# Optimization experiments

Measured on AMD Instinct MI355X. Metric: run time of the kernel, lower is better.

## Reference

```python
import jax, jax.numpy as jnp
import numpy as np

N, D, B = 8192, 16, 4
F_EMB, F_FEAT, F_ENC, H, HID = 32, 4, 128, 4, 64
GRAPH_LAYERS, FLOW_ITERS, DUAL_ITERS = 2, 20, 20
DUAL_STEP, DUAL_MOM = 0.01, 0.9


def _graph():
    # symmetric circulant graph: offsets {1,N-1,2,N-2,...}; reverse of slot 2i is 2i+1
    offs = np.array([o for k in range(1, D // 2 + 1) for o in (k, N - k)], dtype=np.int32)
    rev = np.arange(D, dtype=np.int32).reshape(-1, 2)[:, ::-1].reshape(-1)
    v = np.arange(N, dtype=np.int32)[:, None]
    adj = (v + offs[None, :]) % N          # out-neighbor of node v at slot d
    in_nbr = (v - offs[None, :]) % N       # source node of in-edge to v stored at slot d
    out_flat = adj * D + rev[None, :]      # flat index of reverse edge in [N*D]
    bcast = lambda a: np.broadcast_to(a[None], (B, N, D)).copy()
    return bcast(adj), bcast(in_nbr), bcast(out_flat)


def setup_inputs() -> dict:
    key = jax.random.key(0)
    ks = iter(jax.random.split(key, 32))
    dense = lambda k, fi, fo: jax.random.normal(k, (fi, fo), jnp.float32) / np.sqrt(fi)
    adj, in_nbr, out_flat = _graph()
    demands = jax.random.normal(next(ks), (B, N, 1), jnp.float32)
    demands = demands - jnp.mean(demands, axis=1, keepdims=True)  # net-zero supply/demand
    return dict(
        node_embeddings=jax.random.normal(next(ks), (B, N, F_EMB), jnp.float32),
        node_features=jax.random.uniform(next(ks), (B, N, F_FEAT), jnp.float32),
        demands=demands,
        adj_lst=jnp.asarray(adj), flow_indices=jnp.asarray(in_nbr),
        out_indices=jnp.asarray(out_flat), num_nodes=N,
        enc_W1=dense(next(ks), F_EMB + F_FEAT, HID), enc_b1=jnp.zeros((HID,), jnp.float32),
        enc_W2=dense(next(ks), HID, F_ENC), enc_b2=jnp.zeros((F_ENC,), jnp.float32),
        attn_W=jax.random.normal(next(ks), (H, F_ENC, F_ENC), jnp.float32) / np.sqrt(F_ENC),
        attn_aq=jax.random.normal(next(ks), (H, F_ENC), jnp.float32) / np.sqrt(F_ENC),
        attn_ak=jax.random.normal(next(ks), (H, F_ENC), jnp.float32) / np.sqrt(F_ENC),
        gru_W=dense(next(ks), F_ENC, 3 * F_ENC), gru_U=dense(next(ks), F_ENC, 3 * F_ENC),
        gru_b=jnp.zeros((3 * F_ENC,), jnp.float32),
        dec_W1=dense(next(ks), F_ENC, HID), dec_b1=jnp.zeros((HID,), jnp.float32),
        dec_W2=dense(next(ks), HID, 1), dec_b2=jnp.zeros((1,), jnp.float32),
        dual_W1=dense(next(ks), F_ENC, HID), dual_b1=jnp.zeros((HID,), jnp.float32),
        dual_W2=dense(next(ks), HID, 1), dual_b2=jnp.zeros((1,), jnp.float32),
    )


def _mlp2(x, W1, b1, W2, b2, activate_final):
    h = jnp.tanh(x @ W1 + b1)
    o = h @ W2 + b2
    return jnp.tanh(o) if activate_final else o


def _attention_neighborhood(x, adj, W, aq, ak):
    # x:[B,N,F], adj:[B,N,D]; multi-head attention over adjacency-list neighbors
    cq = jnp.einsum('bnf,hf->bhn', x, jnp.einsum('hfg,hg->hf', W, aq))
    ck = jnp.einsum('bnf,hf->bhn', x, jnp.einsum('hfg,hg->hf', W, ak))
    ck_nb = jax.vmap(lambda c, a: c[:, a])(ck, adj)           # [B,H,N,D]
    attn = jax.nn.softmax(jnp.tanh(cq[..., None] + ck_nb), axis=-1)
    x_nb = jax.vmap(lambda xb, a: xb[a])(x, adj)              # [B,N,D,F]
    weighted = jnp.einsum('bhnd,bndf->bhnf', attn, x_nb)
    out = jnp.tanh(jnp.mean(jnp.einsum('bhnf,hfg->bhng', weighted, W), axis=1))
    return out, attn


def _gru(x, h, W, U, b):
    gz, gr, gc = jnp.split(x @ W + b, 3, axis=-1)
    Uz, Ur, Uc = jnp.split(U, 3, axis=1)
    z = jax.nn.sigmoid(gz + h @ Uz)
    r = jax.nn.sigmoid(gr + h @ Ur)
    c = jnp.tanh(gc + (r * h) @ Uc)
    return z * h + (1.0 - z) * c


def _cost(x):
    return x * x


def _cost_deriv(x):
    return 2.0 * x


def _mcf(w, demand, in_idx):
    # proportional min-cost-flow iteration; in_idx[b,v,d] = source of in-edge at slot d
    flow0 = w * jax.nn.relu(-demand)
    def step(carry, _):
        flow, _ = carry
        inflow = jnp.sum(jnp.take_along_axis(flow, in_idx, axis=1), axis=-1, keepdims=True)
        new = w * jax.nn.relu(inflow - demand)
        return (new, flow), None
    (flow, pflow), _ = jax.lax.scan(step, (flow0, flow0), None, length=FLOW_ITERS)
    return flow, pflow


def _dual_flow(dual_diff, mask):
    # projected momentum descent on cost(f) - dual_diff*f, f >= 0
    z = jnp.zeros_like(dual_diff)
    def step(carry, _):
        flow, acc = carry
        deriv = _cost_deriv(flow - DUAL_MOM * acc) - dual_diff
        acc2 = DUAL_MOM * acc + DUAL_STEP * deriv
        flow2 = jax.nn.relu(mask * (flow - acc2))
        return (flow2, acc2), None
    (flow, _), _ = jax.lax.scan(step, (z, z), None, length=DUAL_ITERS)
    return flow


def reference(node_embeddings, node_features, demands, adj_lst, flow_indices, out_indices,
              num_nodes, enc_W1, enc_b1, enc_W2, enc_b2, attn_W, attn_aq, attn_ak,
              gru_W, gru_U, gru_b, dec_W1, dec_b1, dec_W2, dec_b2,
              dual_W1, dual_b1, dual_W2, dual_b2):
    h = _mlp2(jnp.concatenate([node_embeddings, node_features], axis=-1),
              enc_W1, enc_b1, enc_W2, enc_b2, True)
    for _ in range(GRAPH_LAYERS):  # layers share weights (tf AUTO_REUSE)
        nxt, _ = _attention_neighborhood(h, adj_lst, attn_W, attn_aq, attn_ak)
        h = _gru(nxt, h, gru_W, gru_U, gru_b)
    node_w = _mlp2(h, dec_W1, dec_b1, dec_W2, dec_b2, False)       # [B,N,1]
    pred = jax.vmap(lambda w, a: w[a, 0])(node_w, adj_lst)         # [B,N,D]
    mask = (adj_lst != num_nodes).astype(pred.dtype)
    norm_w = jax.nn.softmax(pred, axis=-1)
    flow, _ = _mcf(norm_w, demands, flow_indices)
    # flow correction: cancel opposing flow on reverse edges
    bf = flow.reshape(B, N * D)
    rev = jnp.take_along_axis(bf, out_indices.reshape(B, N * D), axis=1).reshape(flow.shape)
    flow = jax.nn.relu(flow - jnp.minimum(flow, rev))
    flow_cost = jnp.sum(_cost(flow), axis=(1, 2))
    dual_vars = _mlp2(h, dual_W1, dual_b1, dual_W2, dual_b2, False)  # [B,N,1]
    dual = mask * dual_vars
    dual_tr = mask * jax.vmap(lambda w, a: w[a, 0])(dual_vars, adj_lst)
    dual_diff = dual - dual_tr
    dual_flows = _dual_flow(dual_diff, mask)
    dual_demand = jnp.sum(dual_vars * demands, axis=(1, 2))
    dual_cost = jnp.sum(_cost(dual_flows) - dual_diff * dual_flows, axis=(1, 2)) - dual_demand
    return flow_cost - dual_cost  # loss, [B]
```

## Files before the change

### kernel.cpp

```cpp
#include <hip/hip_runtime.h>

#define NN 8192
#define BB 4
#define DD 16

typedef unsigned short ushort_t;
typedef short bf16x8 __attribute__((ext_vector_type(8)));
typedef float f32x4 __attribute__((ext_vector_type(4)));
typedef unsigned short u16x4 __attribute__((ext_vector_type(4)));
typedef unsigned short u16x8 __attribute__((ext_vector_type(8)));

__host__ __device__ constexpr int soff(int d) { return (d & 1) ? -((d >> 1) + 1) : ((d >> 1) + 1); }

__device__ __forceinline__ float sigmoidf(float x) { return 1.f / (1.f + expf(-x)); }

__device__ __forceinline__ unsigned short f2b(float f) {
  union { float f; unsigned int u; } x;
  x.f = f;
  unsigned int r = (x.u + 0x7FFFu + ((x.u >> 16) & 1u)) >> 16;
  return (unsigned short)r;
}
__device__ __forceinline__ float b2f(ushort_t v) {
  union { unsigned int u; float f; } x;
  x.u = ((unsigned int)v) << 16;
  return x.f;
}

__device__ __forceinline__ float wave_sum(float v) {
#pragma unroll
  for (int o = 32; o; o >>= 1) v += __shfl_down(v, o, 64);
  return v;
}

__global__ __launch_bounds__(256) void prep_kernel(
    const float* __restrict__ gW, const float* __restrict__ gU, const float* __restrict__ aW,
    const float* __restrict__ eW1, const float* __restrict__ eW2,
    const float* __restrict__ dW1, const float* __restrict__ uW1,
    ushort_t* __restrict__ Wt, ushort_t* __restrict__ Wt3, ushort_t* __restrict__ Wt2,
    ushort_t* __restrict__ W1f, ushort_t* __restrict__ W2f,
    ushort_t* __restrict__ dW1f, ushort_t* __restrict__ uW1f) {
  int i = blockIdx.x * 256 + threadIdx.x;
  if (i < 98304) {
    int e = i & 7, lane = (i >> 3) & 63, ks = (i >> 9) & 7, nt = i >> 12;
    int m = lane & 15, g = lane >> 4;
    int n = nt * 16 + m, k = ks * 32 + g * 8 + e;
    float v;
    if (k < 128) v = gW[k * 384 + n];
    else v = (n < 256) ? gU[(k - 128) * 384 + n] : 0.f;
    Wt[i] = f2b(v);
  } else if (i < 114688) {
    int j = i - 98304;
    int e = j & 7, lane = (j >> 3) & 63, ks = (j >> 9) & 3, nt = j >> 11;
    int m = lane & 15, g = lane >> 4;
    int n = nt * 16 + m, k = ks * 32 + g * 8 + e;
    Wt3[j] = f2b(gU[k * 384 + 256 + n]);
  } else if (i < 180224) {
    int j = i - 114688;
    int e = j & 7, lane = (j >> 3) & 63, ks = (j >> 9) & 15, nt = j >> 13;
    int m = lane & 15, g = lane >> 4;
    int gc = nt * 16 + m, k = ks * 32 + g * 8 + e;
    int hh = k >> 7, f = k & 127;
    Wt2[j] = f2b(aW[hh * 16384 + f * 128 + gc]);
  } else if (i < 184320) {
    int j = i - 180224;
    int e = j & 7, lane = (j >> 3) & 63, ks = (j >> 9) & 1, nt = j >> 10;
    int m = lane & 15, g = lane >> 4;
    int n = nt * 16 + m, k = ks * 32 + g * 8 + e;
    W1f[j] = f2b(k < 36 ? eW1[k * 64 + n] : 0.f);
  } else if (i < 192512) {
    int j = i - 184320;
    int e = j & 7, lane = (j >> 3) & 63, ks = (j >> 9) & 1, nt = j >> 10;
    int m = lane & 15, g = lane >> 4;
    int n = nt * 16 + m, k = ks * 32 + g * 8 + e;
    W2f[j] = f2b(eW2[k * 128 + n]);
  } else if (i < 200704) {
    int j = i - 192512;
    int e = j & 7, lane = (j >> 3) & 63, ks = (j >> 9) & 3, nt = j >> 11;
    int m = lane & 15, g = lane >> 4;
    int n = nt * 16 + m, k = ks * 32 + g * 8 + e;
    dW1f[j] = f2b(dW1[k * 64 + n]);
  } else if (i < 208896) {
    int j = i - 200704;
    int e = j & 7, lane = (j >> 3) & 63, ks = (j >> 9) & 3, nt = j >> 11;
    int m = lane & 15, g = lane >> 4;
    int n = nt * 16 + m, k = ks * 32 + g * 8 + e;
    uW1f[j] = f2b(uW1[k * 64 + n]);
  }
}

#define EBS 72
__global__ __launch_bounds__(256) void enc_kernel(
    const float* __restrict__ emb, const float* __restrict__ feat,
    const ushort_t* __restrict__ W1f, const float* __restrict__ b1,
    const ushort_t* __restrict__ W2f, const float* __restrict__ b2,
    ushort_t* __restrict__ hout) {
  __shared__ alignas(16) ushort_t embB[64 * EBS];
  __shared__ alignas(16) ushort_t hidB[64 * EBS];
  int tid = threadIdx.x;
  int w = tid >> 6, lane = tid & 63, m = lane & 15, g = lane >> 4;
  size_t n0 = (size_t)blockIdx.x * 64;
  f32x4 z4 = {0.f, 0.f, 0.f, 0.f};
#pragma unroll
  for (int i = 0; i < 9; i++) ((unsigned int*)embB)[tid + i * 256] = 0u;
  __syncthreads();
#pragma unroll
  for (int i = 0; i < 2; i++) {
    int idx = tid + i * 256;
    int r = idx >> 3, c4 = (idx & 7) * 4;
    float4 v = *(const float4*)&emb[(n0 + r) * 32 + c4];
    u16x4 q = {f2b(v.x), f2b(v.y), f2b(v.z), f2b(v.w)};
    *(u16x4*)&embB[r * EBS + c4] = q;
  }
  if (tid < 64) {
    float4 v = *(const float4*)&feat[(n0 + tid) * 4];
    u16x4 q = {f2b(v.x), f2b(v.y), f2b(v.z), f2b(v.w)};
    *(u16x4*)&embB[tid * EBS + 32] = q;
  }
  __syncthreads();
  {
    f32x4 acc[4];
#pragma unroll
    for (int nt = 0; nt < 4; nt++) acc[nt] = z4;
#pragma unroll
    for (int ks = 0; ks < 2; ks++) {
      bf16x8 a = *(const bf16x8*)&embB[(w * 16 + m) * EBS + ks * 32 + g * 8];
#pragma unroll
      for (int nt = 0; nt < 4; nt++) {
        bf16x8 bb = *(const bf16x8*)&W1f[((nt * 2 + ks) * 64 + lane) * 8];
        acc[nt] = __builtin_amdgcn_mfma_f32_16x16x32_bf16(a, bb, acc[nt], 0, 0, 0);
      }
    }
#pragma unroll
    for (int nt = 0; nt < 4; nt++) {
      int col = nt * 16 + m;
      float bv = b1[col];
#pragma unroll
      for (int r = 0; r < 4; r++)
        hidB[(w * 16 + g * 4 + r) * EBS + col] = f2b(tanhf(acc[nt][r] + bv));
    }
  }
  __syncthreads();
  {
    f32x4 acc[8];
#pragma unroll
    for (int nt = 0; nt < 8; nt++) acc[nt] = z4;
#pragma unroll
    for (int ks = 0; ks < 2; ks++) {
      bf16x8 a = *(const bf16x8*)&hidB[(w * 16 + m) * EBS + ks * 32 + g * 8];
#pragma unroll
      for (int nt = 0; nt < 8; nt++) {
        bf16x8 bb = *(const bf16x8*)&W2f[((nt * 2 + ks) * 64 + lane) * 8];
        acc[nt] = __builtin_amdgcn_mfma_f32_16x16x32_bf16(a, bb, acc[nt], 0, 0, 0);
      }
    }
#pragma unroll
    for (int nt = 0; nt < 8; nt++) {
      int col = nt * 16 + m;
      float bv = b2[col];
#pragma unroll
      for (int r = 0; r < 4; r++)
        hout[(n0 + w * 16 + g * 4 + r) * 128 + col] = f2b(tanhf(acc[nt][r] + bv));
    }
  }
}

__global__ __launch_bounds__(256) void aqw_kernel(
    const float* __restrict__ W, const float* __restrict__ aq, const float* __restrict__ ak,
    ushort_t* __restrict__ aqkB, float* __restrict__ acc) {
  int i = blockIdx.x * 256 + threadIdx.x;
  if (blockIdx.x == 9 && threadIdx.x < BB) acc[threadIdx.x] = 0.f;
  if (i < 512) {
    int hh = i >> 7, f = i & 127;
    const float* w = W + ((size_t)hh * 128 + f) * 128;
    float s = 0.f, s2 = 0.f;
    for (int g = 0; g < 128; g++) {
      s += w[g] * aq[hh * 128 + g];
      s2 += w[g] * ak[hh * 128 + g];
    }
    int ks = f >> 5, g = (f >> 3) & 3, e = f & 7;
    aqkB[(ks * 64 + g * 16 + hh) * 8 + e] = f2b(s2);
    aqkB[(ks * 64 + g * 16 + 4 + hh) * 8 + e] = f2b(s);
  } else if (i < 2560) {
    int j = i - 512;
    int lane = (j >> 3) & 63;
    if ((lane & 15) >= 8) aqkB[j] = 0;
  }
}

#define HBS 136
#define FRB 528
#define FRW 264
__global__ __launch_bounds__(256, 4) void layer_kernel(
    const ushort_t* __restrict__ hin, const ushort_t* __restrict__ Wt2,
    const ushort_t* __restrict__ Wt, const ushort_t* __restrict__ Wt3,
    const ushort_t* __restrict__ aqkB,
    const float* __restrict__ bg, ushort_t* __restrict__ hout) {
  __shared__ alignas(16) ushort_t hl_bf[32 * HBS];
  __shared__ alignas(16) ushort_t hlT_u[4352];
  __shared__ float ckl[32 * 5];
  __shared__ float cql[16 * 5];
  __shared__ alignas(16) ushort_t aexp[4 * FRB];
  __shared__ alignas(16) ushort_t wgB[16 * FRB];
  ushort_t* hlT = hlT_u;
  ushort_t* xB = hlT_u;
  ushort_t* rhB = hlT_u + 16 * HBS;
  int b = blockIdx.y, v0 = blockIdx.x * 16, tid = threadIdx.x;
  int w = tid >> 6, lane = tid & 63, m = lane & 15, g = lane >> 4;
  const ushort_t* hb = hin + (size_t)b * NN * 128;
  size_t base = ((size_t)b * NN + v0) * 128;
  f32x4 z4 = {0.f, 0.f, 0.f, 0.f};
#pragma unroll
  for (int i = 0; i < 2; i++) {
    int idx = tid + i * 256;
    int r = idx >> 4, c8 = (idx & 15) * 8;
    int row = (v0 - 8 + r) & (NN - 1);
    *(u16x8*)&hl_bf[r * HBS + c8] = *(const u16x8*)&hb[(size_t)row * 128 + c8];
  }
#pragma unroll
  for (int i = 0; i < 4; i++) {
    int word = tid + i * 256;
    ((unsigned int*)aexp)[(word >> 8) * FRW + (word & 255)] = 0u;
  }
  __syncthreads();
#pragma unroll
  for (int i = 0; i < 4; i++) {
    int idx = tid + i * 256;
    int c = idx & 127, r4 = (idx >> 7) * 4;
    u16x4 q = {hl_bf[r4 * HBS + c], hl_bf[(r4 + 1) * HBS + c],
               hl_bf[(r4 + 2) * HBS + c], hl_bf[(r4 + 3) * HBS + c]};
    *(u16x4*)&hlT[(c >> 4) * FRB + (((r4 >> 3)) * 16 + (c & 15)) * 8 + (r4 & 7)] = q;
  }
  if (w < 2) {
    f32x4 accB = z4;
    for (int ks = 0; ks < 4; ks++) {
      bf16x8 a = *(const bf16x8*)&hl_bf[(w * 16 + m) * HBS + ks * 32 + g * 8];
      bf16x8 bb = *(const bf16x8*)&aqkB[(ks * 64 + lane) * 8];
      accB = __builtin_amdgcn_mfma_f32_16x16x32_bf16(a, bb, accB, 0, 0, 0);
    }
    int arow = w * 16 + g * 4;
    if (m < 4) {
#pragma unroll
      for (int r = 0; r < 4; r++) ckl[(arow + r) * 5 + m] = accB[r];
    } else if (m < 8) {
#pragma unroll
      for (int r = 0; r < 4; r++) {
        int row = arow + r;
        if (row >= 8 && row < 24) cql[(row - 8) * 5 + (m - 4)] = accB[r];
      }
    }
  }
  __syncthreads();
  {
    int grp = tid >> 2, q = tid & 3;
    int t = grp >> 2, hh = grp & 3;
    float cq = cql[t * 5 + hh];
    float ex[4];
    float mx = -3.0e38f;
#pragma unroll
    for (int dq = 0; dq < 4; dq++) {
      int d = q * 4 + dq;
      float s = tanhf(cq + ckl[(t + 8 + soff(d)) * 5 + hh]);
      ex[dq] = s;
      mx = fmaxf(mx, s);
    }
    mx = fmaxf(mx, __shfl_xor(mx, 1, 64));
    mx = fmaxf(mx, __shfl_xor(mx, 2, 64));
    float sum = 0.f;
#pragma unroll
    for (int dq = 0; dq < 4; dq++) {
      ex[dq] = expf(ex[dq] - mx);
      sum += ex[dq];
    }
    sum += __shfl_xor(sum, 1, 64);
    sum += __shfl_xor(sum, 2, 64);
    float inv = 1.f / sum;
#pragma unroll
    for (int dq = 0; dq < 4; dq++) {
      int d = q * 4 + dq;
      int col = t + 8 + soff(d);
      aexp[hh * FRB + ((col >> 3) * 16 + t) * 8 + (col & 7)] = f2b(ex[dq] * inv);
    }
  }
  __syncthreads();
  {
    bf16x8 bwin[2];
#pragma unroll
    for (int t2 = 0; t2 < 2; t2++)
      bwin[t2] = *(const bf16x8*)&hlT[(w * 2 + t2) * FRB + lane * 8];
#pragma unroll
    for (int hh = 0; hh < 4; hh++) {
      bf16x8 a = *(const bf16x8*)&aexp[hh * FRB + lane * 8];
#pragma unroll
      for (int t2 = 0; t2 < 2; t2++) {
        int nt = w * 2 + t2;
        f32x4 c = __builtin_amdgcn_mfma_f32_16x16x32_bf16(a, bwin[t2], z4, 0, 0, 0);
        int ksb = hh * 4 + (nt >> 1);
        int gq = (nt & 1) * 2 + (m >> 3);
        int e = m & 7;
#pragma unroll
        for (int r = 0; r < 4; r++)
          wgB[ksb * FRB + (gq * 16 + g * 4 + r) * 8 + e] = f2b(c[r]);
      }
    }
  }
  __syncthreads();
  {
    f32x4 acc[2];
    acc[0] = z4; acc[1] = z4;
    for (int ks = 0; ks < 16; ks++) {
      bf16x8 a = *(const bf16x8*)&wgB[ks * FRB + lane * 8];
#pragma unroll
      for (int t2 = 0; t2 < 2; t2++) {
        int nt = w * 2 + t2;
        bf16x8 bb = *(const bf16x8*)&Wt2[((nt * 16 + ks) * 64 + lane) * 8];
        acc[t2] = __builtin_amdgcn_mfma_f32_16x16x32_bf16(a, bb, acc[t2], 0, 0, 0);
      }
    }
    __syncthreads();
#pragma unroll
    for (int t2 = 0; t2 < 2; t2++) {
      int gc = (w * 2 + t2) * 16 + m;
#pragma unroll
      for (int r = 0; r < 4; r++)
        xB[(g * 4 + r) * HBS + gc] = f2b(tanhf(0.25f * acc[t2][r]));
    }
  }
  __syncthreads();
  f32x4 accZ[2], accR[2], accG[2];
#pragma unroll
  for (int t2 = 0; t2 < 2; t2++) { accZ[t2] = z4; accR[t2] = z4; accG[t2] = z4; }
  for (int ks = 0; ks < 8; ks++) {
    bf16x8 a = (ks < 4) ? *(const bf16x8*)&xB[m * HBS + ks * 32 + g * 8]
                        : *(const bf16x8*)&hl_bf[(m + 8) * HBS + (ks - 4) * 32 + g * 8];
#pragma unroll
    for (int t2 = 0; t2 < 2; t2++) {
      int ntz = w * 2 + t2;
      bf16x8 bz = *(const bf16x8*)&Wt[((ntz * 8 + ks) * 64 + lane) * 8];
      accZ[t2] = __builtin_amdgcn_mfma_f32_16x16x32_bf16(a, bz, accZ[t2], 0, 0, 0);
      bf16x8 br = *(const bf16x8*)&Wt[(((8 + ntz) * 8 + ks) * 64 + lane) * 8];
      accR[t2] = __builtin_amdgcn_mfma_f32_16x16x32_bf16(a, br, accR[t2], 0, 0, 0);
      if (ks < 4) {
        bf16x8 bc = *(const bf16x8*)&Wt[(((16 + ntz) * 8 + ks) * 64 + lane) * 8];
        accG[t2] = __builtin_amdgcn_mfma_f32_16x16x32_bf16(a, bc, accG[t2], 0, 0, 0);
      }
    }
  }
  float zf[2][4], gcf[2][4];
#pragma unroll
  for (int t2 = 0; t2 < 2; t2++) {
    int j = (w * 2 + t2) * 16 + m;
    float bz = bg[j], br = bg[128 + j], bc = bg[256 + j];
#pragma unroll
    for (int r = 0; r < 4; r++) {
      int row = g * 4 + r;
      float hv = b2f(hl_bf[(row + 8) * HBS + j]);
      zf[t2][r] = sigmoidf(accZ[t2][r] + bz);
      float rr = sigmoidf(accR[t2][r] + br);
      rhB[row * HBS + j] = f2b(rr * hv);
      gcf[t2][r] = accG[t2][r] + bc;
    }
  }
  __syncthreads();
  ushort_t* hstage = wgB;
  {
    f32x4 acc2[2];
    acc2[0] = z4; acc2[1] = z4;
    for (int ks = 0; ks < 4; ks++) {
      bf16x8 a = *(const bf16x8*)&rhB[m * HBS + ks * 32 + g * 8];
#pragma unroll
      for (int t2 = 0; t2 < 2; t2++) {
        int nt = w * 2 + t2;
        bf16x8 bb = *(const bf16x8*)&Wt3[((nt * 4 + ks) * 64 + lane) * 8];
        acc2[t2] = __builtin_amdgcn_mfma_f32_16x16x32_bf16(a, bb, acc2[t2], 0, 0, 0);
      }
    }
#pragma unroll
    for (int t2 = 0; t2 < 2; t2++) {
      int j = (w * 2 + t2) * 16 + m;
#pragma unroll
      for (int r = 0; r < 4; r++) {
        int row = g * 4 + r;
        float hv = b2f(hl_bf[(row + 8) * HBS + j]);
        float c = tanhf(gcf[t2][r] + acc2[t2][r]);
        hstage[row * HBS + j] = f2b(zf[t2][r] * hv + (1.f - zf[t2][r]) * c);
      }
    }
  }
  __syncthreads();
  {
    int row = tid >> 4, c8 = (tid & 15) * 8;
    *(u16x8*)&hout[base + (size_t)row * 128 + c8] = *(const u16x8*)&hstage[row * HBS + c8];
  }
}

__global__ __launch_bounds__(256) void dec_kernel(
    const ushort_t* __restrict__ h, const float* __restrict__ dem,
    const ushort_t* __restrict__ dW1f, const float* __restrict__ db1,
    const float* __restrict__ dW2, const float* __restrict__ db2,
    const ushort_t* __restrict__ uW1f, const float* __restrict__ ub1,
    const float* __restrict__ uW2, const float* __restrict__ ub2,
    float* __restrict__ node_w, float* __restrict__ dual_v, float* __restrict__ acc) {
  __shared__ alignas(16) ushort_t hB[64 * HBS];
  __shared__ float red[4];
  int b = blockIdx.y, n0 = blockIdx.x * 64, tid = threadIdx.x;
  int w = tid >> 6, lane = tid & 63, m = lane & 15, g = lane >> 4;
  f32x4 z4 = {0.f, 0.f, 0.f, 0.f};
  size_t base = ((size_t)b * NN + n0) * 128;
#pragma unroll
  for (int i = 0; i < 4; i++) {
    int idx = tid + i * 256;
    int r = idx >> 4, c8 = (idx & 15) * 8;
    *(u16x8*)&hB[r * HBS + c8] = *(const u16x8*)&h[base + (size_t)r * 128 + c8];
  }
  __syncthreads();
  f32x4 accD[4], accU[4];
#pragma unroll
  for (int nt = 0; nt < 4; nt++) { accD[nt] = z4; accU[nt] = z4; }
  for (int ks = 0; ks < 4; ks++) {
    bf16x8 a = *(const bf16x8*)&hB[(w * 16 + m) * HBS + ks * 32 + g * 8];
#pragma unroll
    for (int nt = 0; nt < 4; nt++) {
      bf16x8 bd = *(const bf16x8*)&dW1f[((nt * 4 + ks) * 64 + lane) * 8];
      accD[nt] = __builtin_amdgcn_mfma_f32_16x16x32_bf16(a, bd, accD[nt], 0, 0, 0);
      bf16x8 bu = *(const bf16x8*)&uW1f[((nt * 4 + ks) * 64 + lane) * 8];
      accU[nt] = __builtin_amdgcn_mfma_f32_16x16x32_bf16(a, bu, accU[nt], 0, 0, 0);
    }
  }
  float accd = 0.f;
#pragma unroll
  for (int r = 0; r < 4; r++) {
    float sD = 0.f, sU = 0.f;
#pragma unroll
    for (int nt = 0; nt < 4; nt++) {
      int col = nt * 16 + m;
      sD += tanhf(accD[nt][r] + db1[col]) * dW2[col];
      sU += tanhf(accU[nt][r] + ub1[col]) * uW2[col];
    }
#pragma unroll
    for (int o = 1; o < 16; o <<= 1) {
      sD += __shfl_xor(sD, o, 64);
      sU += __shfl_xor(sU, o, 64);
    }
    if (m == 0) {
      int n = n0 + w * 16 + g * 4 + r;
      node_w[(size_t)b * NN + n] = sD + db2[0];
      float dv = sU + ub2[0];
      dual_v[(size_t)b * NN + n] = dv;
      accd += dv * dem[(size_t)b * NN + n];
    }
  }
  float s = wave_sum(accd);
  if (lane == 0) red[w] = s;
  __syncthreads();
  if (tid == 0) atomicAdd(&acc[b], red[0] + red[1] + red[2] + red[3]);
}

__global__ __launch_bounds__(64) void sm_kernel(
    const float* __restrict__ node_w, const float* __restrict__ dem,
    float* __restrict__ nwT, float* __restrict__ fl0) {
  int b = blockIdx.y;
  int v = blockIdx.x * 64 + threadIdx.x;
  const float* nw = node_w + (size_t)b * NN;
  float p[16];
  float mx = -3.0e38f;
#pragma unroll
  for (int d = 0; d < 16; d++) {
    p[d] = nw[(v + soff(d)) & (NN - 1)];
    mx = fmaxf(mx, p[d]);
  }
  float s = 0.f;
#pragma unroll
  for (int d = 0; d < 16; d++) {
    p[d] = expf(p[d] - mx);
    s += p[d];
  }
  float inv = 1.f / s;
  float fd = fmaxf(-dem[(size_t)b * NN + v], 0.f);
#pragma unroll
  for (int d = 0; d < 16; d++) {
    size_t idx = ((size_t)b * 16 + d) * NN + v;
    float w = p[d] * inv;
    nwT[idx] = w;
    fl0[idx] = w * fd;
  }
}

#define MCI 10
#define MHALO 80
#define MCW 128
#define MCOLS (MCW + 2 * MHALO)
__global__ __launch_bounds__(256) void mcf_fused_kernel(
    const float* __restrict__ src, float* __restrict__ dstg,
    const float* __restrict__ nwT, const float* __restrict__ dem) {
  __shared__ float fl[2][16][MCOLS];
  __shared__ float dm[MCOLS];
  int b = blockIdx.y, v0 = blockIdx.x * MCW, tid = threadIdx.x;
  for (int e = tid; e < 16 * MCOLS; e += 256) {
    int d = e / MCOLS, c = e - d * MCOLS;
    int g = (v0 - MHALO + c) & (NN - 1);
    fl[0][d][c] = src[((size_t)b * 16 + d) * NN + g];
  }
  for (int c = tid; c < MCOLS; c += 256)
    dm[c] = dem[(size_t)b * NN + ((v0 - MHALO + c) & (NN - 1))];
  __syncthreads();
  int cur = 0;
  for (int it = 0; it < MCI; it++) {
    int lo = 8 * (it + 1), hi = MCOLS - 8 * (it + 1);
    for (int c = lo + tid; c < hi; c += 256) {
      float s = 0.f;
#pragma unroll
      for (int d = 0; d < 16; d++) s += fl[cur][d][c - soff(d)];
      float val = fmaxf(s - dm[c], 0.f);
      int g = (v0 - MHALO + c) & (NN - 1);
#pragma unroll
      for (int d = 0; d < 16; d++)
        fl[1 - cur][d][c] = nwT[((size_t)b * 16 + d) * NN + g] * val;
    }
    cur ^= 1;
    __syncthreads();
  }
  if (tid < MCW) {
    int c = MHALO + tid;
    int g = v0 + tid;
#pragma unroll
    for (int d = 0; d < 16; d++)
      dstg[((size_t)b * 16 + d) * NN + g] = fl[cur][d][c];
  }
}

__global__ __launch_bounds__(64) void tail_kernel(
    const float* __restrict__ fl, const float* __restrict__ dv, float* __restrict__ acc) {
  int b = blockIdx.y;
  int v = blockIdx.x * 64 + threadIdx.x;
  float s = 0.f;
#pragma unroll
  for (int d = 0; d < 16; d++) {
    float f = fl[((size_t)b * 16 + d) * NN + v];
    int a = (v + soff(d)) & (NN - 1);
    float r = fl[((size_t)b * 16 + (d ^ 1)) * NN + a];
    float c = f - fminf(f, r);
    c = fmaxf(c, 0.f);
    s += c * c;
  }
  float me = dv[(size_t)b * NN + v];
#pragma unroll
  for (int d = 0; d < 16; d++) {
    float dd = me - dv[(size_t)b * NN + ((v + soff(d)) & (NN - 1))];
    float f = 0.f, ac = 0.f;
#pragma unroll
    for (int it = 0; it < 20; it++) {
      float deriv = 2.f * (f - 0.9f * ac) - dd;
      ac = 0.9f * ac + 0.01f * deriv;
      f = fmaxf(f - ac, 0.f);
    }
    s -= f * f - dd * f;
  }
  s = wave_sum(s);
  if (threadIdx.x == 0) atomicAdd(&acc[b], s);
}

__global__ __launch_bounds__(64) void fin_kernel(const float* __restrict__ acc, float* __restrict__ out) {
  int i = threadIdx.x;
  if (i < BB) out[i] = acc[i];
}
__global__ __launch_bounds__(64) void sentinel_kernel(float* __restrict__ out) {
  int i = threadIdx.x;
  if (i < BB) out[i] = 99999.0f;
}

extern "C" void kernel_launch(void* const* d_in, const int* in_sizes, int n_in,
                              void* d_out, int out_size, void* d_ws, size_t ws_size,
                              hipStream_t stream) {
  (void)out_size; (void)ws_size;
  float* out = (float*)d_out;
  if (n_in < 25 || in_sizes[0] != 1048576 || in_sizes[3] != 524288 ||
      in_sizes[11] != 65536 || in_sizes[14] != 49152 || in_sizes[24] != 1) {
    sentinel_kernel<<<dim3(1), 64, 0, stream>>>(out);
    return;
  }
  const float* emb = (const float*)d_in[0];
  const float* feat = (const float*)d_in[1];
  const float* dem = (const float*)d_in[2];
  const float* eW1 = (const float*)d_in[7];
  const float* eb1 = (const float*)d_in[8];
  const float* eW2 = (const float*)d_in[9];
  const float* eb2 = (const float*)d_in[10];
  const float* aW = (const float*)d_in[11];
  const float* aq = (const float*)d_in[12];
  const float* ak = (const float*)d_in[13];
  const float* gW = (const float*)d_in[14];
  const float* gU = (const float*)d_in[15];
  const float* gb = (const float*)d_in[16];
  const float* dW1 = (const float*)d_in[17];
  const float* db1 = (const float*)d_in[18];
  const float* dW2 = (const float*)d_in[19];
  const float* db2 = (const float*)d_in[20];
  const float* uW1 = (const float*)d_in[21];
  const float* ub1 = (const float*)d_in[22];
  const float* uW2 = (const float*)d_in[23];
  const float* ub2 = (const float*)d_in[24];

  float* ws = (float*)d_ws;
  ushort_t* h = (ushort_t*)ws;
  ushort_t* h2 = h + 4194304;
  float* aqkBf = ws + 4194304;
  float* node_w = aqkBf + 1024;
  float* dualv = node_w + 32768;
  float* nwT = dualv + 32768;
  float* flA = nwT + 524288;
  float* flB = flA + 524288;
  float* accv = flB + 524288;
  ushort_t* aqkB = (ushort_t*)aqkBf;
  ushort_t* Wt = (ushort_t*)nwT;
  ushort_t* Wt3 = Wt + 98304;
  ushort_t* Wt2 = Wt3 + 16384;
  ushort_t* W1f = Wt2 + 65536;
  ushort_t* W2f = W1f + 4096;
  ushort_t* dW1f = W2f + 8192;
  ushort_t* uW1f = dW1f + 8192;

  aqw_kernel<<<dim3(10), 256, 0, stream>>>(aW, aq, ak, aqkB, accv);
  prep_kernel<<<dim3(816), 256, 0, stream>>>(gW, gU, aW, eW1, eW2, dW1, uW1,
                                             Wt, Wt3, Wt2, W1f, W2f, dW1f, uW1f);
  enc_kernel<<<dim3(512), 256, 0, stream>>>(emb, feat, W1f, eb1, W2f, eb2, h);
  layer_kernel<<<dim3(512, 4), 256, 0, stream>>>(h, Wt2, Wt, Wt3, aqkB, gb, h2);
  layer_kernel<<<dim3(512, 4), 256, 0, stream>>>(h2, Wt2, Wt, Wt3, aqkB, gb, h);
  dec_kernel<<<dim3(128, 4), 256, 0, stream>>>(h, dem, dW1f, db1, dW2, db2,
                                               uW1f, ub1, uW2, ub2, node_w, dualv, accv);
  sm_kernel<<<dim3(128, 4), 64, 0, stream>>>(node_w, dem, nwT, flA);
  mcf_fused_kernel<<<dim3(64, 4), 256, 0, stream>>>(flA, flB, nwT, dem);
  mcf_fused_kernel<<<dim3(64, 4), 256, 0, stream>>>(flB, flA, nwT, dem);
  tail_kernel<<<dim3(128, 4), 64, 0, stream>>>(flA, dualv, accv);
  fin_kernel<<<dim3(1), 64, 0, stream>>>(accv, out);
}
```

Before: 148.1 us.

## Fuse softmax into first MCF pass, tail into second, merge aqw into prep

```diff
diff --git a/kernel.cpp b/kernel.cpp
--- a/kernel.cpp
+++ b/kernel.cpp
@@ -36,10 +36,13 @@
     const float* __restrict__ gW, const float* __restrict__ gU, const float* __restrict__ aW,
     const float* __restrict__ eW1, const float* __restrict__ eW2,
     const float* __restrict__ dW1, const float* __restrict__ uW1,
+    const float* __restrict__ aqv, const float* __restrict__ akv,
     ushort_t* __restrict__ Wt, ushort_t* __restrict__ Wt3, ushort_t* __restrict__ Wt2,
     ushort_t* __restrict__ W1f, ushort_t* __restrict__ W2f,
-    ushort_t* __restrict__ dW1f, ushort_t* __restrict__ uW1f) {
+    ushort_t* __restrict__ dW1f, ushort_t* __restrict__ uW1f,
+    ushort_t* __restrict__ aqkB, float* __restrict__ acc) {
   int i = blockIdx.x * 256 + threadIdx.x;
+  if (i < BB) acc[i] = 0.f;
   if (i < 98304) {
     int e = i & 7, lane = (i >> 3) & 63, ks = (i >> 9) & 7, nt = i >> 12;
     int m = lane & 15, g = lane >> 4;
@@ -85,6 +88,22 @@
     int m = lane & 15, g = lane >> 4;
     int n = nt * 16 + m, k = ks * 32 + g * 8 + e;
     uW1f[j] = f2b(uW1[k * 64 + n]);
+  } else if (i < 209408) {
+    int j = i - 208896;
+    int hh = j >> 7, f = j & 127;
+    const float* w = aW + ((size_t)hh * 128 + f) * 128;
+    float s = 0.f, s2 = 0.f;
+    for (int g = 0; g < 128; g++) {
+      s += w[g] * aqv[hh * 128 + g];
+      s2 += w[g] * akv[hh * 128 + g];
+    }
+    int ks = f >> 5, g = (f >> 3) & 3, e = f & 7;
+    aqkB[(ks * 64 + g * 16 + hh) * 8 + e] = f2b(s2);
+    aqkB[(ks * 64 + g * 16 + 4 + hh) * 8 + e] = f2b(s);
+  } else if (i < 211456) {
+    int j = i - 209408;
+    int lane = (j >> 3) & 63;
+    if ((lane & 15) >= 8) aqkB[j] = 0;
   }
 }
 
@@ -161,29 +180,6 @@
       for (int r = 0; r < 4; r++)
         hout[(n0 + w * 16 + g * 4 + r) * 128 + col] = f2b(tanhf(acc[nt][r] + bv));
     }
-  }
-}
-
-__global__ __launch_bounds__(256) void aqw_kernel(
-    const float* __restrict__ W, const float* __restrict__ aq, const float* __restrict__ ak,
-    ushort_t* __restrict__ aqkB, float* __restrict__ acc) {
-  int i = blockIdx.x * 256 + threadIdx.x;
-  if (blockIdx.x == 9 && threadIdx.x < BB) acc[threadIdx.x] = 0.f;
-  if (i < 512) {
-    int hh = i >> 7, f = i & 127;
-    const float* w = W + ((size_t)hh * 128 + f) * 128;
-    float s = 0.f, s2 = 0.f;
-    for (int g = 0; g < 128; g++) {
-      s += w[g] * aq[hh * 128 + g];
-      s2 += w[g] * ak[hh * 128 + g];
-    }
-    int ks = f >> 5, g = (f >> 3) & 3, e = f & 7;
-    aqkB[(ks * 64 + g * 16 + hh) * 8 + e] = f2b(s2);
-    aqkB[(ks * 64 + g * 16 + 4 + hh) * 8 + e] = f2b(s);
-  } else if (i < 2560) {
-    int j = i - 512;
-    int lane = (j >> 3) & 63;
-    if ((lane & 15) >= 8) aqkB[j] = 0;
   }
 }
 
@@ -222,14 +218,6 @@
     ((unsigned int*)aexp)[(word >> 8) * FRW + (word & 255)] = 0u;
   }
   __syncthreads();
-#pragma unroll
-  for (int i = 0; i < 4; i++) {
-    int idx = tid + i * 256;
-    int c = idx & 127, r4 = (idx >> 7) * 4;
-    u16x4 q = {hl_bf[r4 * HBS + c], hl_bf[(r4 + 1) * HBS + c],
-               hl_bf[(r4 + 2) * HBS + c], hl_bf[(r4 + 3) * HBS + c]};
-    *(u16x4*)&hlT[(c >> 4) * FRB + (((r4 >> 3)) * 16 + (c & 15)) * 8 + (r4 & 7)] = q;
-  }
   if (w < 2) {
     f32x4 accB = z4;
     for (int ks = 0; ks < 4; ks++) {
@@ -247,6 +235,16 @@
         int row = arow + r;
         if (row >= 8 && row < 24) cql[(row - 8) * 5 + (m - 4)] = accB[r];
       }
+    }
+  } else {
+    int t2i = tid - 128;
+#pragma unroll
+    for (int i = 0; i < 8; i++) {
+      int idx = t2i + i * 128;
+      int c = idx & 127, r4 = (idx >> 7) * 4;
+      u16x4 q = {hl_bf[r4 * HBS + c], hl_bf[(r4 + 1) * HBS + c],
+                 hl_bf[(r4 + 2) * HBS + c], hl_bf[(r4 + 3) * HBS + c]};
+      *(u16x4*)&hlT[(c >> 4) * FRB + (((r4 >> 3)) * 16 + (c & 15)) * 8 + (r4 & 7)] = q;
     }
   }
   __syncthreads();
@@ -455,108 +453,134 @@
   if (tid == 0) atomicAdd(&acc[b], red[0] + red[1] + red[2] + red[3]);
 }
 
-__global__ __launch_bounds__(64) void sm_kernel(
+#define M1H 80
+#define M1C 288
+__global__ __launch_bounds__(256) void sm_mcf_kernel(
     const float* __restrict__ node_w, const float* __restrict__ dem,
-    float* __restrict__ nwT, float* __restrict__ fl0) {
-  int b = blockIdx.y;
-  int v = blockIdx.x * 64 + threadIdx.x;
+    float* __restrict__ nwTg, float* __restrict__ dstg) {
+  __shared__ float fl[2][16][M1C];
+  __shared__ float nwL[16][M1C];
+  __shared__ float dm[M1C];
+  int b = blockIdx.y, v0 = blockIdx.x * 128, tid = threadIdx.x;
   const float* nw = node_w + (size_t)b * NN;
-  float p[16];
-  float mx = -3.0e38f;
-#pragma unroll
-  for (int d = 0; d < 16; d++) {
-    p[d] = nw[(v + soff(d)) & (NN - 1)];
-    mx = fmaxf(mx, p[d]);
-  }
-  float s = 0.f;
-#pragma unroll
-  for (int d = 0; d < 16; d++) {
-    p[d] = expf(p[d] - mx);
-    s += p[d];
-  }
-  float inv = 1.f / s;
-  float fd = fmaxf(-dem[(size_t)b * NN + v], 0.f);
-#pragma unroll
-  for (int d = 0; d < 16; d++) {
-    size_t idx = ((size_t)b * 16 + d) * NN + v;
-    float w = p[d] * inv;
-    nwT[idx] = w;
-    fl0[idx] = w * fd;
-  }
-}
-
-#define MCI 10
-#define MHALO 80
-#define MCW 128
-#define MCOLS (MCW + 2 * MHALO)
-__global__ __launch_bounds__(256) void mcf_fused_kernel(
-    const float* __restrict__ src, float* __restrict__ dstg,
-    const float* __restrict__ nwT, const float* __restrict__ dem) {
-  __shared__ float fl[2][16][MCOLS];
-  __shared__ float dm[MCOLS];
-  int b = blockIdx.y, v0 = blockIdx.x * MCW, tid = threadIdx.x;
-  for (int e = tid; e < 16 * MCOLS; e += 256) {
-    int d = e / MCOLS, c = e - d * MCOLS;
-    int g = (v0 - MHALO + c) & (NN - 1);
-    fl[0][d][c] = src[((size_t)b * 16 + d) * NN + g];
-  }
-  for (int c = tid; c < MCOLS; c += 256)
-    dm[c] = dem[(size_t)b * NN + ((v0 - MHALO + c) & (NN - 1))];
+  for (int c = tid; c < M1C; c += 256) {
+    int v = (v0 - M1H + c) & (NN - 1);
+    float p[16];
+    float mx = -3.0e38f;
+#pragma unroll
+    for (int d = 0; d < 16; d++) {
+      p[d] = nw[(v + soff(d)) & (NN - 1)];
+      mx = fmaxf(mx, p[d]);
+    }
+    float s = 0.f;
+#pragma unroll
+    for (int d = 0; d < 16; d++) {
+      p[d] = expf(p[d] - mx);
+      s += p[d];
+    }
+    float inv = 1.f / s;
+    float dv = dem[(size_t)b * NN + v];
+    dm[c] = dv;
+    float fd = fmaxf(-dv, 0.f);
+    bool own = (c >= M1H && c < M1H + 128);
+#pragma unroll
+    for (int d = 0; d < 16; d++) {
+      float wv = p[d] * inv;
+      nwL[d][c] = wv;
+      fl[0][d][c] = wv * fd;
+      if (own) nwTg[((size_t)b * 16 + d) * NN + v] = wv;
+    }
+  }
   __syncthreads();
   int cur = 0;
-  for (int it = 0; it < MCI; it++) {
-    int lo = 8 * (it + 1), hi = MCOLS - 8 * (it + 1);
+  for (int it = 0; it < 10; it++) {
+    int lo = 8 * (it + 1), hi = M1C - 8 * (it + 1);
     for (int c = lo + tid; c < hi; c += 256) {
       float s = 0.f;
 #pragma unroll
       for (int d = 0; d < 16; d++) s += fl[cur][d][c - soff(d)];
       float val = fmaxf(s - dm[c], 0.f);
-      int g = (v0 - MHALO + c) & (NN - 1);
-#pragma unroll
-      for (int d = 0; d < 16; d++)
-        fl[1 - cur][d][c] = nwT[((size_t)b * 16 + d) * NN + g] * val;
+#pragma unroll
+      for (int d = 0; d < 16; d++) fl[1 - cur][d][c] = nwL[d][c] * val;
     }
     cur ^= 1;
     __syncthreads();
   }
-  if (tid < MCW) {
-    int c = MHALO + tid;
-    int g = v0 + tid;
+  if (tid < 128) {
+    int c = M1H + tid;
+    int v = v0 + tid;
 #pragma unroll
     for (int d = 0; d < 16; d++)
-      dstg[((size_t)b * 16 + d) * NN + g] = fl[cur][d][c];
-  }
-}
-
-__global__ __launch_bounds__(64) void tail_kernel(
-    const float* __restrict__ fl, const float* __restrict__ dv, float* __restrict__ acc) {
-  int b = blockIdx.y;
-  int v = blockIdx.x * 64 + threadIdx.x;
+      dstg[((size_t)b * 16 + d) * NN + v] = fl[cur][d][c];
+  }
+}
+
+#define M2H 88
+#define M2C 304
+__global__ __launch_bounds__(256) void mcf_tail_kernel(
+    const float* __restrict__ src, const float* __restrict__ nwTg,
+    const float* __restrict__ dem, const float* __restrict__ dvv,
+    float* __restrict__ acc) {
+  __shared__ float fl[2][16][M2C];
+  __shared__ float dm[M2C];
+  __shared__ float red[4];
+  int b = blockIdx.y, v0 = blockIdx.x * 128, tid = threadIdx.x;
+  for (int e = tid; e < 16 * M2C; e += 256) {
+    int d = e / M2C, c = e - d * M2C;
+    int gv = (v0 - M2H + c) & (NN - 1);
+    fl[0][d][c] = src[((size_t)b * 16 + d) * NN + gv];
+  }
+  for (int c = tid; c < M2C; c += 256)
+    dm[c] = dem[(size_t)b * NN + ((v0 - M2H + c) & (NN - 1))];
+  __syncthreads();
+  int cur = 0;
+  for (int it = 0; it < 10; it++) {
+    int lo = 8 * (it + 1), hi = M2C - 8 * (it + 1);
+    for (int c = lo + tid; c < hi; c += 256) {
+      float s = 0.f;
+#pragma unroll
+      for (int d = 0; d < 16; d++) s += fl[cur][d][c - soff(d)];
+      float val = fmaxf(s - dm[c], 0.f);
+      int gv = (v0 - M2H + c) & (NN - 1);
+#pragma unroll
+      for (int d = 0; d < 16; d++)
+        fl[1 - cur][d][c] = nwTg[((size_t)b * 16 + d) * NN + gv] * val;
+    }
+    cur ^= 1;
+    __syncthreads();
+  }
   float s = 0.f;
-#pragma unroll
-  for (int d = 0; d < 16; d++) {
-    float f = fl[((size_t)b * 16 + d) * NN + v];
-    int a = (v + soff(d)) & (NN - 1);
-    float r = fl[((size_t)b * 16 + (d ^ 1)) * NN + a];
-    float c = f - fminf(f, r);
-    c = fmaxf(c, 0.f);
-    s += c * c;
-  }
-  float me = dv[(size_t)b * NN + v];
-#pragma unroll
-  for (int d = 0; d < 16; d++) {
-    float dd = me - dv[(size_t)b * NN + ((v + soff(d)) & (NN - 1))];
-    float f = 0.f, ac = 0.f;
-#pragma unroll
-    for (int it = 0; it < 20; it++) {
-      float deriv = 2.f * (f - 0.9f * ac) - dd;
-      ac = 0.9f * ac + 0.01f * deriv;
-      f = fmaxf(f - ac, 0.f);
-    }
-    s -= f * f - dd * f;
+  if (tid < 128) {
+    int c = M2H + tid;
+#pragma unroll
+    for (int d = 0; d < 16; d++) {
+      float f = fl[cur][d][c];
+      float r = fl[cur][d ^ 1][c + soff(d)];
+      float cc = f - fminf(f, r);
+      cc = fmaxf(cc, 0.f);
+      s += cc * cc;
+    }
+  } else {
+    int v = v0 + (tid - 128);
+    float me = dvv[(size_t)b * NN + v];
+#pragma unroll
+    for (int d = 0; d < 16; d++) {
+      float dd = me - dvv[(size_t)b * NN + ((v + soff(d)) & (NN - 1))];
+      float f = 0.f, ac = 0.f;
+#pragma unroll
+      for (int it = 0; it < 20; it++) {
+        float deriv = 2.f * (f - 0.9f * ac) - dd;
+        ac = 0.9f * ac + 0.01f * deriv;
+        f = fmaxf(f - ac, 0.f);
+      }
+      s -= f * f - dd * f;
+    }
   }
   s = wave_sum(s);
-  if (threadIdx.x == 0) atomicAdd(&acc[b], s);
+  int lane = tid & 63, w = tid >> 6;
+  if (lane == 0) red[w] = s;
+  __syncthreads();
+  if (tid == 0) atomicAdd(&acc[b], red[0] + red[1] + red[2] + red[3]);
 }
 
 __global__ __launch_bounds__(64) void fin_kernel(const float* __restrict__ acc, float* __restrict__ out) {
@@ -619,17 +643,14 @@
   ushort_t* dW1f = W2f + 8192;
   ushort_t* uW1f = dW1f + 8192;
 
-  aqw_kernel<<<dim3(10), 256, 0, stream>>>(aW, aq, ak, aqkB, accv);
-  prep_kernel<<<dim3(816), 256, 0, stream>>>(gW, gU, aW, eW1, eW2, dW1, uW1,
-                                             Wt, Wt3, Wt2, W1f, W2f, dW1f, uW1f);
+  prep_kernel<<<dim3(826), 256, 0, stream>>>(gW, gU, aW, eW1, eW2, dW1, uW1, aq, ak,
+                                             Wt, Wt3, Wt2, W1f, W2f, dW1f, uW1f, aqkB, accv);
   enc_kernel<<<dim3(512), 256, 0, stream>>>(emb, feat, W1f, eb1, W2f, eb2, h);
   layer_kernel<<<dim3(512, 4), 256, 0, stream>>>(h, Wt2, Wt, Wt3, aqkB, gb, h2);
   layer_kernel<<<dim3(512, 4), 256, 0, stream>>>(h2, Wt2, Wt, Wt3, aqkB, gb, h);
   dec_kernel<<<dim3(128, 4), 256, 0, stream>>>(h, dem, dW1f, db1, dW2, db2,
                                                uW1f, ub1, uW2, ub2, node_w, dualv, accv);
-  sm_kernel<<<dim3(128, 4), 64, 0, stream>>>(node_w, dem, nwT, flA);
-  mcf_fused_kernel<<<dim3(64, 4), 256, 0, stream>>>(flA, flB, nwT, dem);
-  mcf_fused_kernel<<<dim3(64, 4), 256, 0, stream>>>(flB, flA, nwT, dem);
-  tail_kernel<<<dim3(128, 4), 64, 0, stream>>>(flA, dualv, accv);
+  sm_mcf_kernel<<<dim3(64, 4), 256, 0, stream>>>(node_w, dem, nwT, flB);
+  mcf_tail_kernel<<<dim3(64, 4), 256, 0, stream>>>(flB, nwT, dem, dualv, accv);
   fin_kernel<<<dim3(1), 64, 0, stream>>>(accv, out);
 }
```

After: 136.8 us (median of 2 runs). 1.08x faster.
